# Kernel optimization log

Hardware: AMD Instinct MI355X
Metric: run time of the kernel (lower is better)

## Reference

```python
import jax, jax.numpy as jnp
import numpy as np

H = 2048  # hidden_size
I = 8192  # intermediate_size
B, S = 4, 2048


def setup_inputs() -> dict:
    key = jax.random.key(0)
    ks = jax.random.split(key, 8)
    scale = 1.0 / np.sqrt(H)
    scale_i = 1.0 / np.sqrt(I)
    x = jax.random.normal(ks[0], (B, S, H), dtype=jnp.float32)
    mask = jax.random.randint(ks[1], (B, S), 0, 2) > 0  # bool per-token routing
    # torch nn.Linear weights are [out_features, in_features]
    w1 = jax.random.normal(ks[2], (I, H), dtype=jnp.float32) * scale
    w2 = jax.random.normal(ks[3], (H, I), dtype=jnp.float32) * scale_i
    w3 = jax.random.normal(ks[4], (I, H), dtype=jnp.float32) * scale
    u1 = jax.random.normal(ks[5], (I, H), dtype=jnp.float32) * scale
    u2 = jax.random.normal(ks[6], (H, I), dtype=jnp.float32) * scale_i
    u3 = jax.random.normal(ks[7], (I, H), dtype=jnp.float32) * scale
    return {"x": x, "mask": mask, "w1": w1, "w2": w2, "w3": w3,
            "u1": u1, "u2": u2, "u3": u3}


def reference(x, mask, w1, w2, w3, u1, u2, u3):
    # branch 1 SwiGLU: silu(x @ w1^T) * (x @ w3^T), then w2
    proj1 = jax.nn.silu(jnp.einsum('bsh,ih->bsi', x, w1)) * jnp.einsum('bsh,ih->bsi', x, w3)
    proj2 = jax.nn.silu(jnp.einsum('bsh,ih->bsi', x, u1)) * jnp.einsum('bsh,ih->bsi', x, u3)
    out1 = jnp.einsum('bsi,hi->bsh', proj1, w2)
    out2 = jnp.einsum('bsi,hi->bsh', proj2, u2)
    m = mask[:, :, None]
    return jnp.where(m, out1, out2)
```

## Files before the change

### kernel.cpp

```cpp
#include <hip/hip_runtime.h>
#include <hip/hip_bf16.h>
#include <stdint.h>

#define DIM_H 2048
#define DIM_I 8192
#define TOKENS 8192
#define RBMAX 66

typedef __attribute__((ext_vector_type(8))) short bf16x8;
typedef __attribute__((ext_vector_type(4))) float f32x4;

__device__ __forceinline__ unsigned short f2bf(float f) {
    union { float f; unsigned u; } v; v.f = f;
    unsigned r = (v.u + 0x7FFF + ((v.u >> 16) & 1)) >> 16;
    return (unsigned short)r;
}

__global__ __launch_bounds__(256) void cvt_kernel(const float* __restrict__ in,
                                                  unsigned short* __restrict__ out,
                                                  int n4) {
    int stride = gridDim.x * blockDim.x;
    for (int j = blockIdx.x * blockDim.x + threadIdx.x; j < n4; j += stride) {
        float4 v = reinterpret_cast<const float4*>(in)[j];
        ushort4 o;
        o.x = f2bf(v.x); o.y = f2bf(v.y); o.z = f2bf(v.z); o.w = f2bf(v.w);
        reinterpret_cast<ushort4*>(out)[j] = o;
    }
}

__global__ __launch_bounds__(256) void compact_kernel(const int* __restrict__ mask,
                                                      int* __restrict__ idx,
                                                      int* __restrict__ hdr) {
    __shared__ int cnt[256];
    const int t = threadIdx.x;
    const int base = t * 32;
    unsigned bits = 0;
#pragma unroll
    for (int j = 0; j < 32; ++j)
        if (mask[base + j] != 0) bits |= (1u << j);
    const int c = __popc(bits);
    cnt[t] = c;
    __syncthreads();
    for (int off = 1; off < 256; off <<= 1) {
        int v = cnt[t];
        int add = (t >= off) ? cnt[t - off] : 0;
        __syncthreads();
        cnt[t] = v + add;
        __syncthreads();
    }
    const int Mw  = cnt[255];
    const int MwP = (Mw + 127) & ~127;
    const int Mu  = TOKENS - Mw;
    const int MuP = (Mu + 127) & ~127;
    const int total = MwP + MuP;

    for (int j = t; j < RBMAX * 128; j += 256) idx[j] = -1;
    __syncthreads();

    int pw = cnt[t] - c;
    int pz = base - pw;
#pragma unroll
    for (int j = 0; j < 32; ++j) {
        int tok = base + j;
        if ((bits >> j) & 1) idx[pw++] = tok;
        else                 idx[MwP + pz++] = tok;
    }
    if (t == 0) {
        hdr[0] = MwP >> 7;
        hdr[1] = total >> 7;
        hdr[2] = Mw;
        hdr[3] = Mu;
    }
}

__global__ __launch_bounds__(256, 2) void gemm1_kernel(
    const unsigned short* __restrict__ xb,
    const unsigned short* __restrict__ w1b, const unsigned short* __restrict__ w3b,
    const unsigned short* __restrict__ u1b, const unsigned short* __restrict__ u3b,
    const int* __restrict__ idx, const int* __restrict__ hdr,
    unsigned short* __restrict__ P)
{
    const int wBlocks = hdr[0];
    const int rbTotal = hdr[1];
    const int rb = blockIdx.y;
    if (rb >= rbTotal) return;
    const bool isW = (rb < wBlocks);
    const unsigned short* B1 = isW ? w1b : u1b;
    const unsigned short* B3 = isW ? w3b : u3b;
    const int K = DIM_H, N = DIM_I;

    __shared__ __align__(16) unsigned short sA[128 * 32];
    __shared__ __align__(16) unsigned short sB1[128 * 32];
    __shared__ __align__(16) unsigned short sB3[128 * 32];

    const int t = threadIdx.x;
    const int lane = t & 63;
    const int wave = t >> 6;
    const int wr = wave >> 1, wc = wave & 1;
    const int bm0 = rb * 128;
    const int bn0 = blockIdx.x * 128;

    f32x4 acc1[4][4] = {};
    f32x4 acc3[4][4] = {};

    const int srow = t >> 2;
    const int scol = (t & 3) << 3;
    int r0 = idx[bm0 + srow];       if (r0 < 0) r0 = 0;
    int r1 = idx[bm0 + srow + 64];  if (r1 < 0) r1 = 0;
    const unsigned short* ga0 = xb + (size_t)r0 * K + scol;
    const unsigned short* ga1 = xb + (size_t)r1 * K + scol;
    const unsigned short* gb1 = B1 + (size_t)(bn0 + srow) * K + scol;
    const unsigned short* gb3 = B3 + (size_t)(bn0 + srow) * K + scol;
    const int ldsbase = wave << 9;

    const int frow = lane & 15;
    const int fk0  = (lane >> 4) << 3;

    for (int kt = 0; kt < K; kt += 32) {
        __syncthreads();
#define GLL1(dst, src, it) \
        __builtin_amdgcn_global_load_lds( \
            (const __attribute__((address_space(1))) void*)((src) + kt), \
            (__attribute__((address_space(3))) void*)&(dst)[(it) * 2048 + ldsbase], 16, 0, 0)
#define GLLB(dst, src, it) \
        __builtin_amdgcn_global_load_lds( \
            (const __attribute__((address_space(1))) void*)((src) + (size_t)(it) * 64 * K + kt), \
            (__attribute__((address_space(3))) void*)&(dst)[(it) * 2048 + ldsbase], 16, 0, 0)
        GLL1(sA, ga0, 0); GLL1(sA, ga1, 1);
        GLLB(sB1, gb1, 0); GLLB(sB1, gb1, 1);
        GLLB(sB3, gb3, 0); GLLB(sB3, gb3, 1);
#undef GLL1
#undef GLLB
        __syncthreads();

        bf16x8 af[4], b1f[4], b3f[4];
#pragma unroll
        for (int m = 0; m < 4; ++m)
            af[m] = *reinterpret_cast<const bf16x8*>(&sA[(wr * 64 + m * 16 + frow) * 32 + fk0]);
#pragma unroll
        for (int n = 0; n < 4; ++n) {
            b1f[n] = *reinterpret_cast<const bf16x8*>(&sB1[(wc * 64 + n * 16 + frow) * 32 + fk0]);
            b3f[n] = *reinterpret_cast<const bf16x8*>(&sB3[(wc * 64 + n * 16 + frow) * 32 + fk0]);
        }
#pragma unroll
        for (int m = 0; m < 4; ++m)
#pragma unroll
            for (int n = 0; n < 4; ++n) {
                acc1[m][n] = __builtin_amdgcn_mfma_f32_16x16x32_bf16(af[m], b1f[n], acc1[m][n], 0, 0, 0);
                acc3[m][n] = __builtin_amdgcn_mfma_f32_16x16x32_bf16(af[m], b3f[n], acc3[m][n], 0, 0, 0);
            }
    }

    const int crow0 = (lane >> 4) * 4;
    const int ccol  = lane & 15;
#pragma unroll
    for (int m = 0; m < 4; ++m) {
#pragma unroll
        for (int n = 0; n < 4; ++n) {
#pragma unroll
            for (int r = 0; r < 4; ++r) {
                float h1 = acc1[m][n][r];
                float h3 = acc3[m][n][r];
                float sig = 1.0f / (1.0f + __expf(-h1));
                float p = h1 * sig * h3;
                size_t row = (size_t)(bm0 + wr * 64 + m * 16 + crow0 + r);
                size_t col = (size_t)(bn0 + wc * 64 + n * 16 + ccol);
                P[row * (size_t)N + col] = f2bf(p);
            }
        }
    }
}

__global__ __launch_bounds__(256, 2) void gemm2_kernel(
    const unsigned short* __restrict__ P,
    const unsigned short* __restrict__ w2b, const unsigned short* __restrict__ u2b,
    const int* __restrict__ idx, const int* __restrict__ hdr,
    float* __restrict__ out)
{
    const int wBlocks = hdr[0];
    const int rbTotal = hdr[1];
    const int rb = blockIdx.y;
    if (rb >= rbTotal) return;
    const unsigned short* B = (rb < wBlocks) ? w2b : u2b;
    const int K = DIM_I, N = DIM_H;

    __shared__ __align__(16) unsigned short sA[128 * 32];
    __shared__ __align__(16) unsigned short sB[128 * 32];

    const int t = threadIdx.x;
    const int lane = t & 63;
    const int wave = t >> 6;
    const int wr = wave >> 1, wc = wave & 1;
    const int bm0 = rb * 128;
    const int bn0 = blockIdx.x * 128;

    f32x4 acc[4][4] = {};

    const int srow = t >> 2;
    const int scol = (t & 3) << 3;
    const unsigned short* ga = P + (size_t)(bm0 + srow) * K + scol;
    const unsigned short* gb = B + (size_t)(bn0 + srow) * K + scol;
    const int ldsbase = wave << 9;

    const int frow = lane & 15;
    const int fk0  = (lane >> 4) << 3;

    for (int kt = 0; kt < K; kt += 32) {
        __syncthreads();
#define GLL(dst, src, it) \
        __builtin_amdgcn_global_load_lds( \
            (const __attribute__((address_space(1))) void*)((src) + (size_t)(it) * 64 * K + kt), \
            (__attribute__((address_space(3))) void*)&(dst)[(it) * 2048 + ldsbase], 16, 0, 0)
        GLL(sA, ga, 0); GLL(sA, ga, 1);
        GLL(sB, gb, 0); GLL(sB, gb, 1);
#undef GLL
        __syncthreads();

        bf16x8 af[4], bf[4];
#pragma unroll
        for (int m = 0; m < 4; ++m)
            af[m] = *reinterpret_cast<const bf16x8*>(&sA[(wr * 64 + m * 16 + frow) * 32 + fk0]);
#pragma unroll
        for (int n = 0; n < 4; ++n)
            bf[n] = *reinterpret_cast<const bf16x8*>(&sB[(wc * 64 + n * 16 + frow) * 32 + fk0]);
#pragma unroll
        for (int m = 0; m < 4; ++m)
#pragma unroll
            for (int n = 0; n < 4; ++n)
                acc[m][n] = __builtin_amdgcn_mfma_f32_16x16x32_bf16(af[m], bf[n], acc[m][n], 0, 0, 0);
    }

    const int crow0 = (lane >> 4) * 4;
    const int ccol  = lane & 15;
#pragma unroll
    for (int m = 0; m < 4; ++m) {
#pragma unroll
        for (int r = 0; r < 4; ++r) {
            int rowc = bm0 + wr * 64 + m * 16 + crow0 + r;
            int g = idx[rowc];
            if (g >= 0) {
#pragma unroll
                for (int n = 0; n < 4; ++n) {
                    size_t col = (size_t)(bn0 + wc * 64 + n * 16 + ccol);
                    out[(size_t)g * (size_t)N + col] = acc[m][n][r];
                }
            }
        }
    }
}

extern "C" void kernel_launch(void* const* d_in, const int* in_sizes, int n_in,
                              void* d_out, int out_size, void* d_ws, size_t ws_size,
                              hipStream_t stream) {
    const float* x    = (const float*)d_in[0];
    const int*   mask = (const int*)d_in[1];
    const float* w1 = (const float*)d_in[2];
    const float* w2 = (const float*)d_in[3];
    const float* w3 = (const float*)d_in[4];
    const float* u1 = (const float*)d_in[5];
    const float* u2 = (const float*)d_in[6];
    const float* u3 = (const float*)d_in[7];
    float* out = (float*)d_out;

    const size_t XN = (size_t)TOKENS * DIM_H;
    const size_t WN = (size_t)DIM_I * DIM_H;
    const size_t PN = (size_t)(RBMAX * 128) * DIM_I;

    unsigned short* ws = (unsigned short*)d_ws;
    unsigned short* xb = ws;
    unsigned short* P  = xb + XN;
    unsigned short* s0 = P + PN;
    unsigned short* s1 = s0 + WN;
    unsigned short* s2 = s1 + WN;
    unsigned short* s3 = s2 + WN;
    int* idx = (int*)(s3 + WN);
    int* hdr = idx + RBMAX * 128;

    const int cvtBlocks = 2048;
    const int n4 = (int)(WN / 4);

    cvt_kernel<<<cvtBlocks, 256, 0, stream>>>(x,  xb, (int)(XN / 4));
    cvt_kernel<<<cvtBlocks, 256, 0, stream>>>(w1, s0, n4);
    cvt_kernel<<<cvtBlocks, 256, 0, stream>>>(w3, s1, n4);
    cvt_kernel<<<cvtBlocks, 256, 0, stream>>>(u1, s2, n4);
    cvt_kernel<<<cvtBlocks, 256, 0, stream>>>(u3, s3, n4);
    compact_kernel<<<1, 256, 0, stream>>>(mask, idx, hdr);

    gemm1_kernel<<<dim3(DIM_I / 128, RBMAX), 256, 0, stream>>>(
        xb, s0, s1, s2, s3, idx, hdr, P);

    cvt_kernel<<<cvtBlocks, 256, 0, stream>>>(w2, s0, n4);
    cvt_kernel<<<cvtBlocks, 256, 0, stream>>>(u2, s1, n4);

    gemm2_kernel<<<dim3(DIM_H / 128, RBMAX), 256, 0, stream>>>(
        P, s0, s1, idx, hdr, out);
}
```

Measured before the change: 1.219 ms.

## Rewrite GEMMs as 256x256 tiles with LDS double-buffering and interleaved W1/W3

Both GEMMs now use 256x256 tiles with 512 threads. A software-pipelined K loop prefetches into double-buffered, XOR-swizzled LDS through global_load_lds, and the MFMA blocks are raised in priority with setprio. W1 and W3 are fused into one interleaved weight matrix during conversion, so gemm1 runs a single B operand stream and the SwiGLU pairs land in adjacent accumulators. The grid is swizzled for L2 locality and token compaction pads to 256 rows. This aims to cut global/LDS traffic per FLOP and hide load latency, at the cost of more padding waste and a large shared-memory footprint that limits occupancy.

```diff
diff --git a/kernel.cpp b/kernel.cpp
--- a/kernel.cpp
+++ b/kernel.cpp
@@ -5,15 +5,17 @@
 #define DIM_H 2048
 #define DIM_I 8192
 #define TOKENS 8192
-#define RBMAX 66
+#define RB256 34
+#define CROWS (RB256*256)
 
 typedef __attribute__((ext_vector_type(8))) short bf16x8;
 typedef __attribute__((ext_vector_type(4))) float f32x4;
 
+#define MF(a,b,c) __builtin_amdgcn_mfma_f32_16x16x32_bf16((a),(b),(c),0,0,0)
+
 __device__ __forceinline__ unsigned short f2bf(float f) {
     union { float f; unsigned u; } v; v.f = f;
-    unsigned r = (v.u + 0x7FFF + ((v.u >> 16) & 1)) >> 16;
-    return (unsigned short)r;
+    return (unsigned short)((v.u + 0x7FFF + ((v.u >> 16) & 1)) >> 16);
 }
 
 __global__ __launch_bounds__(256) void cvt_kernel(const float* __restrict__ in,
@@ -25,6 +27,26 @@
         ushort4 o;
         o.x = f2bf(v.x); o.y = f2bf(v.y); o.z = f2bf(v.z); o.w = f2bf(v.w);
         reinterpret_cast<ushort4*>(out)[j] = o;
+    }
+}
+
+__global__ __launch_bounds__(256) void cvt13_kernel(const float* __restrict__ w1,
+                                                    const float* __restrict__ w3,
+                                                    unsigned short* __restrict__ W13,
+                                                    int n4) {
+    int stride = gridDim.x * blockDim.x;
+    for (int j = blockIdx.x * blockDim.x + threadIdx.x; j < n4; j += stride) {
+        int flat = j << 2;
+        int R = flat >> 11;
+        int col = flat & 2047;
+        int orow = ((R >> 4) << 5) | (R & 15);
+        float4 v1 = reinterpret_cast<const float4*>(w1)[j];
+        float4 v3 = reinterpret_cast<const float4*>(w3)[j];
+        ushort4 o1, o3;
+        o1.x=f2bf(v1.x); o1.y=f2bf(v1.y); o1.z=f2bf(v1.z); o1.w=f2bf(v1.w);
+        o3.x=f2bf(v3.x); o3.y=f2bf(v3.y); o3.z=f2bf(v3.z); o3.w=f2bf(v3.w);
+        *reinterpret_cast<ushort4*>(&W13[(size_t)orow * DIM_H + col]) = o1;
+        *reinterpret_cast<ushort4*>(&W13[(size_t)(orow + 16) * DIM_H + col]) = o3;
     }
 }
 
@@ -49,12 +71,11 @@
         __syncthreads();
     }
     const int Mw  = cnt[255];
-    const int MwP = (Mw + 127) & ~127;
+    const int MwP = (Mw + 255) & ~255;
     const int Mu  = TOKENS - Mw;
-    const int MuP = (Mu + 127) & ~127;
-    const int total = MwP + MuP;
-
-    for (int j = t; j < RBMAX * 128; j += 256) idx[j] = -1;
+    const int MuP = (Mu + 255) & ~255;
+
+    for (int j = t; j < CROWS; j += 256) idx[j] = -1;
     __syncthreads();
 
     int pw = cnt[t] - c;
@@ -66,184 +87,197 @@
         else                 idx[MwP + pz++] = tok;
     }
     if (t == 0) {
-        hdr[0] = MwP >> 7;
-        hdr[1] = total >> 7;
+        hdr[0] = MwP >> 8;
+        hdr[1] = (MwP + MuP) >> 8;
         hdr[2] = Mw;
         hdr[3] = Mu;
     }
 }
 
-__global__ __launch_bounds__(256, 2) void gemm1_kernel(
+
+#define LDA4(BASE, KS, MQ) do { \
+    const unsigned short* _sl = &smem[(BASE) + (KS)*8192]; \
+    af0 = *reinterpret_cast<const bf16x8*>(&_sl[(rAb + (MQ)*64 +  0)*32 + c16r]); \
+    af1 = *reinterpret_cast<const bf16x8*>(&_sl[(rAb + (MQ)*64 + 16)*32 + c16r]); \
+    af2 = *reinterpret_cast<const bf16x8*>(&_sl[(rAb + (MQ)*64 + 32)*32 + c16r]); \
+    af3 = *reinterpret_cast<const bf16x8*>(&_sl[(rAb + (MQ)*64 + 48)*32 + c16r]); \
+} while(0)
+
+#define LDB4(BASE, KS) do { \
+    const unsigned short* _sl = &smem[(BASE) + 16384 + (KS)*8192]; \
+    bfr0 = *reinterpret_cast<const bf16x8*>(&_sl[(rBb +  0)*32 + c16r]); \
+    bfr1 = *reinterpret_cast<const bf16x8*>(&_sl[(rBb + 16)*32 + c16r]); \
+    bfr2 = *reinterpret_cast<const bf16x8*>(&_sl[(rBb + 32)*32 + c16r]); \
+    bfr3 = *reinterpret_cast<const bf16x8*>(&_sl[(rBb + 48)*32 + c16r]); \
+} while(0)
+
+#define STAGE2(UB_, S0_, S1_, KOFS_) do { \
+    __builtin_amdgcn_global_load_lds((const __attribute__((address_space(1))) void*)((S0_) + (KOFS_)), \
+        (__attribute__((address_space(3))) void*)&smem[(UB_) + wave*512], 16, 0, 0); \
+    __builtin_amdgcn_global_load_lds((const __attribute__((address_space(1))) void*)((S1_) + (KOFS_)), \
+        (__attribute__((address_space(3))) void*)&smem[(UB_) + 4096 + wave*512], 16, 0, 0); \
+} while(0)
+
+#define MFMA16(M0) do { \
+    acc[M0+0][0]=MF(af0,bfr0,acc[M0+0][0]); acc[M0+0][1]=MF(af0,bfr1,acc[M0+0][1]); \
+    acc[M0+0][2]=MF(af0,bfr2,acc[M0+0][2]); acc[M0+0][3]=MF(af0,bfr3,acc[M0+0][3]); \
+    acc[M0+1][0]=MF(af1,bfr0,acc[M0+1][0]); acc[M0+1][1]=MF(af1,bfr1,acc[M0+1][1]); \
+    acc[M0+1][2]=MF(af1,bfr2,acc[M0+1][2]); acc[M0+1][3]=MF(af1,bfr3,acc[M0+1][3]); \
+    acc[M0+2][0]=MF(af2,bfr0,acc[M0+2][0]); acc[M0+2][1]=MF(af2,bfr1,acc[M0+2][1]); \
+    acc[M0+2][2]=MF(af2,bfr2,acc[M0+2][2]); acc[M0+2][3]=MF(af2,bfr3,acc[M0+2][3]); \
+    acc[M0+3][0]=MF(af3,bfr0,acc[M0+3][0]); acc[M0+3][1]=MF(af3,bfr1,acc[M0+3][1]); \
+    acc[M0+3][2]=MF(af3,bfr2,acc[M0+3][2]); acc[M0+3][3]=MF(af3,bfr3,acc[M0+3][3]); \
+} while(0)
+
+#define BARMFMA(M0) do { \
+    __builtin_amdgcn_s_barrier(); \
+    asm volatile("s_waitcnt lgkmcnt(0)" ::: "memory"); \
+    __builtin_amdgcn_sched_barrier(0); \
+    __builtin_amdgcn_s_setprio(1); \
+    MFMA16(M0); \
+    __builtin_amdgcn_s_setprio(0); \
+    __builtin_amdgcn_s_barrier(); \
+} while(0)
+
+#define KLOOP(NT) do { \
+    STAGE2(0,             sa0, sa1, 0);   STAGE2(16384,         sb0, sb1, 0); \
+    STAGE2(8192,          sa0, sa1, 32);  STAGE2(16384 + 8192,  sb0, sb1, 32); \
+    STAGE2(32768,         sa0, sa1, 64);  STAGE2(32768 + 16384, sb0, sb1, 64); \
+    asm volatile("s_waitcnt vmcnt(4)" ::: "memory"); \
+    __builtin_amdgcn_s_barrier(); \
+    for (int t = 0; t < (NT); ++t) { \
+        const int cur = (t & 1) << 15; \
+        const int nxt = cur ^ 32768; \
+        const int k1o = ((t + 1 < (NT)) ? t + 1 : t) * 64 + 32; \
+        const int k2o = ((t + 2 < (NT)) ? t + 2 : t) * 64; \
+        LDA4(cur, 0, 0); LDB4(cur, 0); STAGE2(nxt + 8192,  sa0, sa1, k1o); BARMFMA(0); \
+        LDA4(cur, 0, 1);               STAGE2(nxt + 24576, sb0, sb1, k1o); BARMFMA(4); \
+        LDA4(cur, 1, 0); LDB4(cur, 1); STAGE2(cur,         sa0, sa1, k2o); BARMFMA(0); \
+        LDA4(cur, 1, 1);               STAGE2(cur + 16384, sb0, sb1, k2o); \
+        asm volatile("s_waitcnt vmcnt(4)" ::: "memory"); \
+        BARMFMA(4); \
+    } \
+} while(0)
+
+__global__ __launch_bounds__(512, 2) void gemm1_kernel(
     const unsigned short* __restrict__ xb,
-    const unsigned short* __restrict__ w1b, const unsigned short* __restrict__ w3b,
-    const unsigned short* __restrict__ u1b, const unsigned short* __restrict__ u3b,
+    const unsigned short* __restrict__ W13,
+    const unsigned short* __restrict__ U13,
     const int* __restrict__ idx, const int* __restrict__ hdr,
     unsigned short* __restrict__ P)
 {
-    const int wBlocks = hdr[0];
-    const int rbTotal = hdr[1];
-    const int rb = blockIdx.y;
-    if (rb >= rbTotal) return;
-    const bool isW = (rb < wBlocks);
-    const unsigned short* B1 = isW ? w1b : u1b;
-    const unsigned short* B3 = isW ? w3b : u3b;
-    const int K = DIM_H, N = DIM_I;
-
-    __shared__ __align__(16) unsigned short sA[128 * 32];
-    __shared__ __align__(16) unsigned short sB1[128 * 32];
-    __shared__ __align__(16) unsigned short sB3[128 * 32];
-
-    const int t = threadIdx.x;
-    const int lane = t & 63;
-    const int wave = t >> 6;
-    const int wr = wave >> 1, wc = wave & 1;
-    const int bm0 = rb * 128;
-    const int bn0 = blockIdx.x * 128;
-
-    f32x4 acc1[4][4] = {};
-    f32x4 acc3[4][4] = {};
-
-    const int srow = t >> 2;
-    const int scol = (t & 3) << 3;
-    int r0 = idx[bm0 + srow];       if (r0 < 0) r0 = 0;
-    int r1 = idx[bm0 + srow + 64];  if (r1 < 0) r1 = 0;
-    const unsigned short* ga0 = xb + (size_t)r0 * K + scol;
-    const unsigned short* ga1 = xb + (size_t)r1 * K + scol;
-    const unsigned short* gb1 = B1 + (size_t)(bn0 + srow) * K + scol;
-    const unsigned short* gb3 = B3 + (size_t)(bn0 + srow) * K + scol;
-    const int ldsbase = wave << 9;
-
-    const int frow = lane & 15;
-    const int fk0  = (lane >> 4) << 3;
-
-    for (int kt = 0; kt < K; kt += 32) {
-        __syncthreads();
-#define GLL1(dst, src, it) \
-        __builtin_amdgcn_global_load_lds( \
-            (const __attribute__((address_space(1))) void*)((src) + kt), \
-            (__attribute__((address_space(3))) void*)&(dst)[(it) * 2048 + ldsbase], 16, 0, 0)
-#define GLLB(dst, src, it) \
-        __builtin_amdgcn_global_load_lds( \
-            (const __attribute__((address_space(1))) void*)((src) + (size_t)(it) * 64 * K + kt), \
-            (__attribute__((address_space(3))) void*)&(dst)[(it) * 2048 + ldsbase], 16, 0, 0)
-        GLL1(sA, ga0, 0); GLL1(sA, ga1, 1);
-        GLLB(sB1, gb1, 0); GLLB(sB1, gb1, 1);
-        GLLB(sB3, gb3, 0); GLLB(sB3, gb3, 1);
-#undef GLL1
-#undef GLLB
-        __syncthreads();
-
-        bf16x8 af[4], b1f[4], b3f[4];
-#pragma unroll
-        for (int m = 0; m < 4; ++m)
-            af[m] = *reinterpret_cast<const bf16x8*>(&sA[(wr * 64 + m * 16 + frow) * 32 + fk0]);
-#pragma unroll
-        for (int n = 0; n < 4; ++n) {
-            b1f[n] = *reinterpret_cast<const bf16x8*>(&sB1[(wc * 64 + n * 16 + frow) * 32 + fk0]);
-            b3f[n] = *reinterpret_cast<const bf16x8*>(&sB3[(wc * 64 + n * 16 + frow) * 32 + fk0]);
-        }
-#pragma unroll
-        for (int m = 0; m < 4; ++m)
-#pragma unroll
-            for (int n = 0; n < 4; ++n) {
-                acc1[m][n] = __builtin_amdgcn_mfma_f32_16x16x32_bf16(af[m], b1f[n], acc1[m][n], 0, 0, 0);
-                acc3[m][n] = __builtin_amdgcn_mfma_f32_16x16x32_bf16(af[m], b3f[n], acc3[m][n], 0, 0, 0);
-            }
-    }
-
-    const int crow0 = (lane >> 4) * 4;
-    const int ccol  = lane & 15;
-#pragma unroll
-    for (int m = 0; m < 4; ++m) {
-#pragma unroll
-        for (int n = 0; n < 4; ++n) {
+    __shared__ __align__(16) unsigned short smem[65536];
+    const int wB  = hdr[0];
+    const int rbT = hdr[1];
+    const int nwg = gridDim.x;
+    const int q8  = nwg >> 3;
+    const int swz = ((int)blockIdx.x & 7) * q8 + ((int)blockIdx.x >> 3);
+    const int bx = swz & 63;
+    const int rb = swz >> 6;
+    if (rb >= rbT) return;
+    const unsigned short* Bm = (rb < wB) ? W13 : U13;
+    const int bm0 = rb << 8;
+    const int bn0 = bx << 8;
+
+    const int tid  = threadIdx.x;
+    const int lane = tid & 63;
+    const int wave = tid >> 6;
+    const int wrM = wave >> 2;
+    const int wcN = wave & 3;
+    const int rAb = wrM * 128 + (lane & 15);
+    const int rBb = wcN * 64 + (lane & 15);
+    const int c16r = (((lane >> 4) ^ ((lane >> 1) & 3))) << 3;
+
+    const int p0 = tid, p1 = 512 + tid;
+    const int r0 = p0 >> 2, r1 = p1 >> 2;
+    const int c0 = ((p0 & 3) ^ ((r0 >> 1) & 3)) << 3;
+    const int c1 = ((p1 & 3) ^ ((r1 >> 1) & 3)) << 3;
+    int t0 = idx[bm0 + r0]; if (t0 < 0) t0 = 0;
+    int t1 = idx[bm0 + r1]; if (t1 < 0) t1 = 0;
+    const unsigned short* sa0 = xb + (size_t)t0 * DIM_H + c0;
+    const unsigned short* sa1 = xb + (size_t)t1 * DIM_H + c1;
+    const unsigned short* sb0 = Bm + (size_t)(bn0 + r0) * DIM_H + c0;
+    const unsigned short* sb1 = Bm + (size_t)(bn0 + r1) * DIM_H + c1;
+
+    f32x4 acc[8][4] = {};
+    bf16x8 af0, af1, af2, af3, bfr0, bfr1, bfr2, bfr3;
+
+    KLOOP(32);
+
+    const int crow = (lane >> 4) << 2;
+    const int ccol = lane & 15;
+    unsigned short* Pw = P + (size_t)(bm0 + wrM * 128) * DIM_I
+                           + (size_t)bx * 128 + wcN * 32 + ccol;
+#pragma unroll
+    for (int m = 0; m < 8; ++m) {
+#pragma unroll
+        for (int q = 0; q < 2; ++q) {
+            f32x4 h1 = acc[m][2 * q];
+            f32x4 h3 = acc[m][2 * q + 1];
 #pragma unroll
             for (int r = 0; r < 4; ++r) {
-                float h1 = acc1[m][n][r];
-                float h3 = acc3[m][n][r];
-                float sig = 1.0f / (1.0f + __expf(-h1));
-                float p = h1 * sig * h3;
-                size_t row = (size_t)(bm0 + wr * 64 + m * 16 + crow0 + r);
-                size_t col = (size_t)(bn0 + wc * 64 + n * 16 + ccol);
-                P[row * (size_t)N + col] = f2bf(p);
+                float a = h1[r];
+                float p = a * (1.0f / (1.0f + __expf(-a))) * h3[r];
+                Pw[(size_t)(m * 16 + crow + r) * DIM_I + q * 16] = f2bf(p);
             }
         }
     }
 }
 
-__global__ __launch_bounds__(256, 2) void gemm2_kernel(
+__global__ __launch_bounds__(512, 2) void gemm2_kernel(
     const unsigned short* __restrict__ P,
     const unsigned short* __restrict__ w2b, const unsigned short* __restrict__ u2b,
     const int* __restrict__ idx, const int* __restrict__ hdr,
     float* __restrict__ out)
 {
-    const int wBlocks = hdr[0];
-    const int rbTotal = hdr[1];
-    const int rb = blockIdx.y;
-    if (rb >= rbTotal) return;
-    const unsigned short* B = (rb < wBlocks) ? w2b : u2b;
-    const int K = DIM_I, N = DIM_H;
-
-    __shared__ __align__(16) unsigned short sA[128 * 32];
-    __shared__ __align__(16) unsigned short sB[128 * 32];
-
-    const int t = threadIdx.x;
-    const int lane = t & 63;
-    const int wave = t >> 6;
-    const int wr = wave >> 1, wc = wave & 1;
-    const int bm0 = rb * 128;
-    const int bn0 = blockIdx.x * 128;
-
-    f32x4 acc[4][4] = {};
-
-    const int srow = t >> 2;
-    const int scol = (t & 3) << 3;
-    const unsigned short* ga = P + (size_t)(bm0 + srow) * K + scol;
-    const unsigned short* gb = B + (size_t)(bn0 + srow) * K + scol;
-    const int ldsbase = wave << 9;
-
-    const int frow = lane & 15;
-    const int fk0  = (lane >> 4) << 3;
-
-    for (int kt = 0; kt < K; kt += 32) {
-        __syncthreads();
-#define GLL(dst, src, it) \
-        __builtin_amdgcn_global_load_lds( \
-            (const __attribute__((address_space(1))) void*)((src) + (size_t)(it) * 64 * K + kt), \
-            (__attribute__((address_space(3))) void*)&(dst)[(it) * 2048 + ldsbase], 16, 0, 0)
-        GLL(sA, ga, 0); GLL(sA, ga, 1);
-        GLL(sB, gb, 0); GLL(sB, gb, 1);
-#undef GLL
-        __syncthreads();
-
-        bf16x8 af[4], bf[4];
-#pragma unroll
-        for (int m = 0; m < 4; ++m)
-            af[m] = *reinterpret_cast<const bf16x8*>(&sA[(wr * 64 + m * 16 + frow) * 32 + fk0]);
-#pragma unroll
-        for (int n = 0; n < 4; ++n)
-            bf[n] = *reinterpret_cast<const bf16x8*>(&sB[(wc * 64 + n * 16 + frow) * 32 + fk0]);
-#pragma unroll
-        for (int m = 0; m < 4; ++m)
-#pragma unroll
-            for (int n = 0; n < 4; ++n)
-                acc[m][n] = __builtin_amdgcn_mfma_f32_16x16x32_bf16(af[m], bf[n], acc[m][n], 0, 0, 0);
-    }
-
-    const int crow0 = (lane >> 4) * 4;
-    const int ccol  = lane & 15;
-#pragma unroll
-    for (int m = 0; m < 4; ++m) {
+    __shared__ __align__(16) unsigned short smem[65536];
+    const int wB  = hdr[0];
+    const int rbT = hdr[1];
+    const int nwg = gridDim.x;
+    const int q8  = nwg >> 3;
+    const int swz = ((int)blockIdx.x & 7) * q8 + ((int)blockIdx.x >> 3);
+    const int bx = swz & 7;
+    const int rb = swz >> 3;
+    if (rb >= rbT) return;
+    const unsigned short* Bm = (rb < wB) ? w2b : u2b;
+    const int bm0 = rb << 8;
+    const int bn0 = bx << 8;
+
+    const int tid  = threadIdx.x;
+    const int lane = tid & 63;
+    const int wave = tid >> 6;
+    const int wrM = wave >> 2;
+    const int wcN = wave & 3;
+    const int rAb = wrM * 128 + (lane & 15);
+    const int rBb = wcN * 64 + (lane & 15);
+    const int c16r = (((lane >> 4) ^ ((lane >> 1) & 3))) << 3;
+
+    const int p0 = tid, p1 = 512 + tid;
+    const int r0 = p0 >> 2, r1 = p1 >> 2;
+    const int c0 = ((p0 & 3) ^ ((r0 >> 1) & 3)) << 3;
+    const int c1 = ((p1 & 3) ^ ((r1 >> 1) & 3)) << 3;
+    const unsigned short* sa0 = P  + (size_t)(bm0 + r0) * DIM_I + c0;
+    const unsigned short* sa1 = P  + (size_t)(bm0 + r1) * DIM_I + c1;
+    const unsigned short* sb0 = Bm + (size_t)(bn0 + r0) * DIM_I + c0;
+    const unsigned short* sb1 = Bm + (size_t)(bn0 + r1) * DIM_I + c1;
+
+    f32x4 acc[8][4] = {};
+    bf16x8 af0, af1, af2, af3, bfr0, bfr1, bfr2, bfr3;
+
+    KLOOP(128);
+
+    const int crow = (lane >> 4) << 2;
+    const int ccol = lane & 15;
+#pragma unroll
+    for (int m = 0; m < 8; ++m) {
 #pragma unroll
         for (int r = 0; r < 4; ++r) {
-            int rowc = bm0 + wr * 64 + m * 16 + crow0 + r;
+            int rowc = bm0 + wrM * 128 + m * 16 + crow + r;
             int g = idx[rowc];
             if (g >= 0) {
-#pragma unroll
-                for (int n = 0; n < 4; ++n) {
-                    size_t col = (size_t)(bn0 + wc * 64 + n * 16 + ccol);
-                    out[(size_t)g * (size_t)N + col] = acc[m][n][r];
-                }
+                float* op = out + (size_t)g * DIM_H + bn0 + wcN * 64 + ccol;
+#pragma unroll
+                for (int n = 0; n < 4; ++n) op[n * 16] = acc[m][n][r];
             }
         }
     }
@@ -262,36 +296,33 @@
     const float* u3 = (const float*)d_in[7];
     float* out = (float*)d_out;
 
-    const size_t XN = (size_t)TOKENS * DIM_H;
-    const size_t WN = (size_t)DIM_I * DIM_H;
-    const size_t PN = (size_t)(RBMAX * 128) * DIM_I;
-
-    unsigned short* ws = (unsigned short*)d_ws;
-    unsigned short* xb = ws;
-    unsigned short* P  = xb + XN;
-    unsigned short* s0 = P + PN;
-    unsigned short* s1 = s0 + WN;
-    unsigned short* s2 = s1 + WN;
-    unsigned short* s3 = s2 + WN;
-    int* idx = (int*)(s3 + WN);
-    int* hdr = idx + RBMAX * 128;
+    const size_t XN   = (size_t)TOKENS * DIM_H;
+    const size_t WN   = (size_t)DIM_I * DIM_H;
+    const size_t PN   = (size_t)CROWS * DIM_I;
+    const size_t W13N = 2 * WN;
+
+    unsigned short* ws  = (unsigned short*)d_ws;
+    unsigned short* xb  = ws;
+    unsigned short* Pb  = xb + XN;
+    unsigned short* W13 = Pb + PN;
+    unsigned short* U13 = W13 + W13N;
+    int* idx = (int*)(U13 + W13N);
+    int* hdr = idx + CROWS;
+    unsigned short* w2b = W13;
+    unsigned short* u2b = U13;
 
     const int cvtBlocks = 2048;
     const int n4 = (int)(WN / 4);
 
-    cvt_kernel<<<cvtBlocks, 256, 0, stream>>>(x,  xb, (int)(XN / 4));
-    cvt_kernel<<<cvtBlocks, 256, 0, stream>>>(w1, s0, n4);
-    cvt_kernel<<<cvtBlocks, 256, 0, stream>>>(w3, s1, n4);
-    cvt_kernel<<<cvtBlocks, 256, 0, stream>>>(u1, s2, n4);
-    cvt_kernel<<<cvtBlocks, 256, 0, stream>>>(u3, s3, n4);
+    cvt_kernel  <<<cvtBlocks, 256, 0, stream>>>(x, xb, (int)(XN / 4));
+    cvt13_kernel<<<cvtBlocks, 256, 0, stream>>>(w1, w3, W13, n4);
+    cvt13_kernel<<<cvtBlocks, 256, 0, stream>>>(u1, u3, U13, n4);
     compact_kernel<<<1, 256, 0, stream>>>(mask, idx, hdr);
 
-    gemm1_kernel<<<dim3(DIM_I / 128, RBMAX), 256, 0, stream>>>(
-        xb, s0, s1, s2, s3, idx, hdr, P);
-
-    cvt_kernel<<<cvtBlocks, 256, 0, stream>>>(w2, s0, n4);
-    cvt_kernel<<<cvtBlocks, 256, 0, stream>>>(u2, s1, n4);
-
-    gemm2_kernel<<<dim3(DIM_H / 128, RBMAX), 256, 0, stream>>>(
-        P, s0, s1, idx, hdr, out);
-}
+    gemm1_kernel<<<64 * RB256, 512, 0, stream>>>(xb, W13, U13, idx, hdr, Pb);
+
+    cvt_kernel<<<cvtBlocks, 256, 0, stream>>>(w2, w2b, n4);
+    cvt_kernel<<<cvtBlocks, 256, 0, stream>>>(u2, u2b, n4);
+
+    gemm2_kernel<<<8 * RB256, 512, 0, stream>>>(Pb, w2b, u2b, idx, hdr, out);
+}
```

After: 1.087 ms. 1.12x faster.
